# Performance work log

Hardware: AMD Instinct MI355X
Metric: run time of the kernel (lower is better)

Reference implementation:

```python
import jax, jax.numpy as jnp
import numpy as np
from jax import lax

L, E, H, V, B, S = 25, 64, 8, 30000, 1000, 512


def setup_inputs() -> dict:
    key = jax.random.key(0)
    ks = jax.random.split(key, 24)
    p = lambda k, shape: (jax.random.normal(k, shape) * 0.1).astype(jnp.float32)
    inp = {
        "x": jax.random.randint(ks[0], (B, S), 0, V),
        "embedding": p(ks[1], (V, E)),
        # layer 0 (input dim = E)
        "W_xz0": p(ks[2], (E, H)), "W_hz0": p(ks[3], (H, H)), "b_z0": p(ks[4], (H,)),
        "W_xr0": p(ks[5], (E, H)), "W_hr0": p(ks[6], (H, H)), "b_r0": p(ks[7], (H,)),
        "W_xH0": p(ks[8], (E, H)), "W_rH0": p(ks[9], (H, H)), "b_H0": p(ks[10], (H,)),
        # layers 1..L-1 stacked (input dim = H)
        "W_xz": p(ks[11], (L - 1, H, H)), "W_hz": p(ks[12], (L - 1, H, H)), "b_z": p(ks[13], (L - 1, H)),
        "W_xr": p(ks[14], (L - 1, H, H)), "W_hr": p(ks[15], (L - 1, H, H)), "b_r": p(ks[16], (L - 1, H)),
        "W_xH": p(ks[17], (L - 1, H, H)), "W_rH": p(ks[18], (L - 1, H, H)), "b_H": p(ks[19], (L - 1, H)),
        "W_hy": p(ks[20], (H, 1)), "b_y": p(ks[21], (1,)),
    }
    return inp


def _cell(x_t, h, Wxz, Whz, bz, Wxr, Whr, br, WxH, WrH, bH):
    z = jax.nn.sigmoid(x_t @ Wxz + h @ Whz + bz)
    r = jax.nn.sigmoid(x_t @ Wxr + h @ Whr + br)
    Hc = jnp.tanh(x_t @ WxH + (h * r) @ WrH + bH)
    return h * (1.0 - z) + z * Hc


def reference(x, embedding, W_xz0, W_hz0, b_z0, W_xr0, W_hr0, b_r0, W_xH0, W_rH0, b_H0,
              W_xz, W_hz, b_z, W_xr, W_hr, b_r, W_xH, W_rH, b_H, W_hy, b_y):
    emb = embedding[x]                     # [B, S, E]
    bsz = x.shape[0]
    h0 = jnp.zeros((L, bsz, H), dtype=embedding.dtype)

    def time_step(h_all, x_t):            # h_all: [L, B, H]; x_t: [B, E]
        h_new0 = _cell(x_t, h_all[0], W_xz0, W_hz0, b_z0, W_xr0, W_hr0, b_r0, W_xH0, W_rH0, b_H0)

        def layer_step(inp_t, ws):
            Wxz, Whz, bz, Wxr, Whr, br, WxH, WrH, bH, h_prev = ws
            h_new = _cell(inp_t, h_prev, Wxz, Whz, bz, Wxr, Whr, br, WxH, WrH, bH)
            return h_new, h_new

        _, h_rest = lax.scan(layer_step, h_new0,
                             (W_xz, W_hz, b_z, W_xr, W_hr, b_r, W_xH, W_rH, b_H, h_all[1:]))
        return jnp.concatenate([h_new0[None], h_rest], axis=0), None

    h_last, _ = lax.scan(time_step, h0, jnp.swapaxes(emb, 0, 1))  # scan over S
    logits = h_last[-1] @ W_hy + b_y       # [B, 1]
    return logits.squeeze(-1), h_last
```

## Files before the change

### kernel.cpp

```cpp
#include <hip/hip_runtime.h>
#include <hip/hip_bf16.h>
#include <stdint.h>

#define L_ 25
#define E_ 64
#define H_ 8
#define B_ 1000
#define S_ 512
#define GQ 4
#define NCELL (L_ * GQ)
#define TPBR (NCELL * 8)
#define TS 4
#define NSUPER (S_ / TS + L_ - 1)
#define HS 12
#define XG 36

typedef float v2f __attribute__((ext_vector_type(2)));
typedef float v4f __attribute__((ext_vector_type(4)));

#define PIN(x) asm volatile("" : "+v"(x))

__device__ __forceinline__ v2f pkfma(v2f a, v2f b, v2f c) {
  v2f d;
  asm("v_pk_fma_f32 %0, %1, %2, %3" : "=v"(d) : "v"(a), "v"(b), "v"(c));
  return d;
}
__device__ __forceinline__ v2f pkfma_l(v2f a, v2f b, v2f c) {
  v2f d;
  asm("v_pk_fma_f32 %0, %1, %2, %3 op_sel:[0,0,0] op_sel_hi:[0,1,1]"
      : "=v"(d) : "v"(a), "v"(b), "v"(c));
  return d;
}
__device__ __forceinline__ v2f pkfma_h(v2f a, v2f b, v2f c) {
  v2f d;
  asm("v_pk_fma_f32 %0, %1, %2, %3 op_sel:[1,0,0] op_sel_hi:[1,1,1]"
      : "=v"(d) : "v"(a), "v"(b), "v"(c));
  return d;
}
__device__ __forceinline__ v2f pkadd(v2f a, v2f b) {
  v2f d;
  asm("v_pk_add_f32 %0, %1, %2" : "=v"(d) : "v"(a), "v"(b));
  return d;
}
__device__ __forceinline__ v2f vlo(v4f v) { return __builtin_shufflevector(v, v, 0, 1); }
__device__ __forceinline__ v2f vhi(v4f v) { return __builtin_shufflevector(v, v, 2, 3); }
__device__ __forceinline__ v2f mk2(float a, float b) { v2f r; r.x = a; r.y = b; return r; }

#define CHAIN8(acc, ma, mb, w)            \
  acc = pkfma_l(vlo(ma), w[0], acc);      \
  acc = pkfma_h(vlo(ma), w[1], acc);      \
  acc = pkfma_l(vhi(ma), w[2], acc);      \
  acc = pkfma_h(vhi(ma), w[3], acc);      \
  acc = pkfma_l(vlo(mb), w[4], acc);      \
  acc = pkfma_h(vlo(mb), w[5], acc);      \
  acc = pkfma_l(vhi(mb), w[6], acc);      \
  acc = pkfma_h(vhi(mb), w[7], acc);

#define CHAIN4P(acc, ma, mb, w)           \
  acc = pkfma(vlo(ma), w[0], acc);        \
  acc = pkfma(vhi(ma), w[1], acc);        \
  acc = pkfma(vlo(mb), w[2], acc);        \
  acc = pkfma(vhi(mb), w[3], acc);

__device__ __forceinline__ float ulo(uint32_t u) { return __uint_as_float(u << 16); }
__device__ __forceinline__ float uhi(uint32_t u) { return __uint_as_float(u & 0xffff0000u); }

__device__ __forceinline__ float toF(float v) { return v; }
__device__ __forceinline__ float toF(__hip_bfloat16 v) { return __bfloat162float(v); }
__device__ __forceinline__ void stP(float* p, float v) { *p = v; }
__device__ __forceinline__ void stP(__hip_bfloat16* p, float v) { *p = __float2bfloat16(v); }

__device__ __forceinline__ v2f loadC2(const float* p) { return *(const v2f*)p; }
__device__ __forceinline__ v2f loadC2(const __hip_bfloat16* p) {
  const uint32_t u = *(const uint32_t*)p;
  return mk2(ulo(u), uhi(u));
}

__device__ __forceinline__ void load8f(const __hip_bfloat16* p, float* o) {
  const uint4 v = *(const uint4*)p;
  o[0] = ulo(v.x); o[1] = uhi(v.x); o[2] = ulo(v.y); o[3] = uhi(v.y);
  o[4] = ulo(v.z); o[5] = uhi(v.z); o[6] = ulo(v.w); o[7] = uhi(v.w);
}
__device__ __forceinline__ void load8f(const float* p, float* o) {
  const float4 a = ((const float4*)p)[0];
  const float4 b = ((const float4*)p)[1];
  o[0] = a.x; o[1] = a.y; o[2] = a.z; o[3] = a.w;
  o[4] = b.x; o[5] = b.y; o[6] = b.z; o[7] = b.w;
}

__device__ __forceinline__ void st4(float* p, float a, float b, float c, float d) {
  float4 v; v.x = a; v.y = b; v.z = c; v.w = d;
  *(float4*)p = v;
}
__device__ __forceinline__ void st4(__hip_bfloat16* p, float a, float b, float c, float d) {
  __hip_bfloat16 t[4] = {__float2bfloat16(a), __float2bfloat16(b),
                         __float2bfloat16(c), __float2bfloat16(d)};
  *(ushort4*)p = *(ushort4*)t;
}

__device__ __forceinline__ float sigmo(float x) {
  return __builtin_amdgcn_rcpf(1.f + __expf(-x));
}

__device__ __forceinline__ void detect64(const unsigned short* __restrict__ u,
                                         int tid, float* fl) {
  if (tid < 64) {
    float m = 0.f;
#pragma unroll
    for (int k = 0; k < 4; ++k) {
      const uint32_t q = u[tid * 4 + k];
      float v = fabsf(__uint_as_float(q << 16));
      if (!(v < 1e30f)) v = 1e30f;
      m = fmaxf(m, v);
    }
#pragma unroll
    for (int off = 32; off; off >>= 1) m = fmaxf(m, __shfl_down(m, off, 64));
    if (tid == 0) *fl = (m > 2.0f) ? 0.f : 1.f;
  }
}

template <typename T, typename PT>
__device__ __forceinline__ void pre_body(
    const int* __restrict__ x, const void* __restrict__ embv,
    const void* __restrict__ Wzv, const void* __restrict__ Wrv,
    const void* __restrict__ Whv, PT* __restrict__ pre,
    float* WL, float* TBb) {
  const T* emb = (const T*)embv;
  const T* Wz = (const T*)Wzv;
  const T* Wr = (const T*)Wrv;
  const T* Wh = (const T*)Whv;
  const int tid = threadIdx.x;

  for (int idx = tid; idx < 64 * 24; idx += 256) {
    const int k = idx / 24, c = idx - k * 24;
    float w;
    if (c < 16) w = toF(((c & 1) ? Wr : Wz)[k * 8 + (c >> 1)]);
    else        w = toF(Wh[k * 8 + (c - 16)]);
    WL[idx] = w;
  }
  __syncthreads();

  const int tok = blockIdx.x * 256 + tid;
  const int t = x[tok];

  v2f acc[12];
#pragma unroll
  for (int q = 0; q < 12; ++q) acc[q] = mk2(0.f, 0.f);

  for (int kb = 0; kb < 8; ++kb) {
    float e[8];
    load8f(emb + (size_t)t * E_ + kb * 8, e);
#pragma unroll
    for (int k8 = 0; k8 < 8; ++k8) {
      const v4f* wr = (const v4f*)(WL + (kb * 8 + k8) * 24);
      const v2f ee = mk2(e[k8], e[k8]);
#pragma unroll
      for (int q = 0; q < 6; ++q) {
        const v4f w4 = wr[q];
        acc[2 * q]     = pkfma(ee, vlo(w4), acc[2 * q]);
        acc[2 * q + 1] = pkfma(ee, vhi(w4), acc[2 * q + 1]);
      }
    }
  }

  const int wid = tid >> 6, lane = tid & 63;
  float* tb = TBb + wid * (24 * 65);
#pragma unroll
  for (int q = 0; q < 12; ++q) {
    tb[(2 * q) * 65 + lane] = acc[q].x;
    tb[(2 * q + 1) * 65 + lane] = acc[q].y;
  }
  asm volatile("s_waitcnt lgkmcnt(0)" ::: "memory");
  __builtin_amdgcn_wave_barrier();

  PT* ob = pre + (size_t)(blockIdx.x * 256 + wid * 64) * 24;
#pragma unroll
  for (int it = 0; it < 6; ++it) {
    const int F0 = it * 256 + lane * 4;
    float o[4];
#pragma unroll
    for (int e2 = 0; e2 < 4; ++e2) {
      const int F = F0 + e2;
      const int tk = F / 24;
      const int c = F - tk * 24;
      o[e2] = tb[c * 65 + tk];
    }
    st4(ob + F0, o[0], o[1], o[2], o[3]);
  }
}

template <typename PT>
__global__ __launch_bounds__(256, 4) void gru_pre(
    const int* __restrict__ x, const void* __restrict__ emb,
    const void* __restrict__ Wz, const void* __restrict__ Wr,
    const void* __restrict__ Wh, PT* __restrict__ pre) {
  __shared__ __align__(16) float WL[64 * 24];
  __shared__ __align__(16) float TB[4][24 * 65];
  __shared__ float fl;
  detect64((const unsigned short*)emb, threadIdx.x, &fl);
  __syncthreads();
  if (fl != 0.f) pre_body<__hip_bfloat16, PT>(x, emb, Wz, Wr, Wh, pre, WL, &TB[0][0]);
  else           pre_body<float, PT>(x, emb, Wz, Wr, Wh, pre, WL, &TB[0][0]);
}

#define TIMESTEP(hprev, axK, ahK, slot, hnout)                       \
  {                                                                  \
    const v4f h01_ = ((const v4f*)hgw)[0];                           \
    const v4f h23_ = ((const v4f*)hgw)[1];                           \
    v2f azrh_ = bzr;                                                 \
    CHAIN8(azrh_, h01_, h23_, wzrh);                                 \
    const v2f azr_ = pkadd(azrh_, axK);                              \
    const float r_ = sigmo(azr_.y);                                  \
    *hrgj = (hprev) * r_;                                            \
    __builtin_amdgcn_wave_barrier();                                 \
    const v4f r01_ = ((const v4f*)hrg)[0];                           \
    const v4f r23_ = ((const v4f*)hrg)[1];                           \
    CHAIN4P(ahK, r01_, r23_, wrh2);                                  \
    const float ah_ = ahK.x + ahK.y;                                 \
    const float ez_ = __expf(fminf(-azr_.x, 30.f));                  \
    const float eh_ = __expf(fminf(-2.f * ah_, 30.f));               \
    const float t_ = (hprev) * ez_;                                  \
    const float num_ = fmaf(eh_, t_ - 1.f, t_ + 1.f);                \
    const float den_ = (1.f + ez_) * (1.f + eh_);                    \
    hnout = num_ * __builtin_amdgcn_rcpf(den_);                      \
    *hgwj = hnout;                                                   \
    xc[(slot) * 8 + j] = hnout;                                      \
    __builtin_amdgcn_wave_barrier();                                 \
  }

template <typename T, typename PT>
__device__ __forceinline__ void rec_body(
    const PT* __restrict__ pre,
    const void* __restrict__ Whz0v, const void* __restrict__ bz0v,
    const void* __restrict__ Whr0v, const void* __restrict__ br0v,
    const void* __restrict__ WrH0v, const void* __restrict__ bH0v,
    const void* __restrict__ Wxzv, const void* __restrict__ Whzv,
    const void* __restrict__ bzv, const void* __restrict__ Wxrv,
    const void* __restrict__ Whrv, const void* __restrict__ brv,
    const void* __restrict__ WxHv, const void* __restrict__ WrHv,
    const void* __restrict__ bHv, const void* __restrict__ Whyv,
    const void* __restrict__ byv, void* __restrict__ outv,
    float* hsh, float* hrsh, float* xbuf) {
  const T* Whz0 = (const T*)Whz0v; const T* bz0 = (const T*)bz0v;
  const T* Whr0 = (const T*)Whr0v; const T* br0 = (const T*)br0v;
  const T* WrH0 = (const T*)WrH0v; const T* bH0 = (const T*)bH0v;
  const T* Wxz = (const T*)Wxzv;   const T* Whz = (const T*)Whzv;
  const T* bz = (const T*)bzv;     const T* Wxr = (const T*)Wxrv;
  const T* Whr = (const T*)Whrv;   const T* br = (const T*)brv;
  const T* WxH = (const T*)WxHv;   const T* WrH = (const T*)WrHv;
  const T* bH = (const T*)bHv;     const T* Why = (const T*)Whyv;
  const T* by = (const T*)byv;     T* out = (T*)outv;

  const int tid = threadIdx.x;
  const int gi = tid >> 3;
  const int j = tid & 7;
  const int l = gi >> 2;
  const int g = gi & 3;
  const int b = blockIdx.x * GQ + g;

  for (int i = tid; i < NCELL * HS; i += TPBR) { hsh[i] = 0.f; hrsh[i] = 0.f; }
  for (int i = tid; i < 2 * NCELL * XG; i += TPBR) xbuf[i] = 0.f;

  v2f wzrx[8], wzrh[8], wxh2[4], wrh2[4], bzr;
  float vbh;
  if (l == 0) {
#pragma unroll
    for (int k = 0; k < 8; ++k) {
      wzrh[k] = mk2(toF(Whz0[k * 8 + j]), toF(Whr0[k * 8 + j]));
      wzrx[k] = mk2(0.f, 0.f);
    }
#pragma unroll
    for (int q = 0; q < 4; ++q) {
      wrh2[q] = mk2(toF(WrH0[(2 * q) * 8 + j]), toF(WrH0[(2 * q + 1) * 8 + j]));
      wxh2[q] = mk2(0.f, 0.f);
    }
    bzr = mk2(toF(bz0[j]), toF(br0[j]));
    vbh = toF(bH0[j]);
  } else {
    const int base = (l - 1) * 64;
#pragma unroll
    for (int k = 0; k < 8; ++k) {
      wzrx[k] = mk2(toF(Wxz[base + k * 8 + j]), toF(Wxr[base + k * 8 + j]));
      wzrh[k] = mk2(toF(Whz[base + k * 8 + j]), toF(Whr[base + k * 8 + j]));
    }
#pragma unroll
    for (int q = 0; q < 4; ++q) {
      wxh2[q] = mk2(toF(WxH[base + (2 * q) * 8 + j]), toF(WxH[base + (2 * q + 1) * 8 + j]));
      wrh2[q] = mk2(toF(WrH[base + (2 * q) * 8 + j]), toF(WrH[base + (2 * q + 1) * 8 + j]));
    }
    bzr = mk2(toF(bz[(l - 1) * 8 + j]), toF(br[(l - 1) * 8 + j]));
    vbh = toF(bH[(l - 1) * 8 + j]);
  }
#pragma unroll
  for (int k = 0; k < 8; ++k) { PIN(wzrx[k]); PIN(wzrh[k]); }
#pragma unroll
  for (int q = 0; q < 4; ++q) { PIN(wxh2[q]); PIN(wrh2[q]); }
  PIN(bzr); PIN(vbh);

  const PT* ppr = pre + (size_t)b * (S_ * 24);
  v2f czr0 = mk2(0.f, 0.f), czr1 = czr0, czr2 = czr0, czr3 = czr0;
  float ch0 = 0.f, ch1 = 0.f, ch2 = 0.f, ch3 = 0.f;
  if (l == 0) {
    czr0 = loadC2(ppr + 0 * 24 + 2 * j);  ch0 = toF(ppr[0 * 24 + 16 + j]);
    czr1 = loadC2(ppr + 1 * 24 + 2 * j);  ch1 = toF(ppr[1 * 24 + 16 + j]);
    czr2 = loadC2(ppr + 2 * 24 + 2 * j);  ch2 = toF(ppr[2 * 24 + 16 + j]);
    czr3 = loadC2(ppr + 3 * 24 + 2 * j);  ch3 = toF(ppr[3 * 24 + 16 + j]);
  }

  float* hgw = hsh + gi * HS;
  float* hrg = hrsh + gi * HS;
  float* hgwj = hgw + j;
  float* hrgj = hrg + j;
  const int gp = (gi >= GQ) ? (gi - GQ) * XG : 0;
  const float* xpe = xbuf + NCELL * XG + gp;
  const float* xpo = xbuf + gp;
  float* xce = xbuf + gi * XG;
  float* xco = xbuf + NCELL * XG + gi * XG;

  float hown = 0.f;

  __syncthreads();

  for (int s = 0; s < NSUPER; ++s) {
    const unsigned rel = (unsigned)(s - l);
    if (rel < (unsigned)(S_ / TS)) {
      const float* xp = (s & 1) ? xpo : xpe;
      float* xc = (s & 1) ? xco : xce;

      const v4f xa0 = ((const v4f*)xp)[0];
      const v4f xb0 = ((const v4f*)xp)[1];
      const v4f xa1 = ((const v4f*)xp)[2];
      const v4f xb1 = ((const v4f*)xp)[3];

      v2f nzr0 = mk2(0.f, 0.f), nzr1 = nzr0, nzr2 = nzr0, nzr3 = nzr0;
      float nh0 = 0.f, nh1 = 0.f, nh2 = 0.f, nh3 = 0.f;
      const bool pf = (l == 0) && (rel + 1u < (unsigned)(S_ / TS));
      if (pf) {
        const PT* pn = ppr + (TS * rel + 4) * 24;
        nzr0 = loadC2(pn + 0 * 24 + 2 * j);  nh0 = toF(pn[0 * 24 + 16 + j]);
        nzr1 = loadC2(pn + 1 * 24 + 2 * j);  nh1 = toF(pn[1 * 24 + 16 + j]);
        nzr2 = loadC2(pn + 2 * 24 + 2 * j);  nh2 = toF(pn[2 * 24 + 16 + j]);
        nzr3 = loadC2(pn + 3 * 24 + 2 * j);  nh3 = toF(pn[3 * 24 + 16 + j]);
      }

      v2f ax0 = czr0; CHAIN8(ax0, xa0, xb0, wzrx);
      v2f ah0 = mk2(ch0, vbh); CHAIN4P(ah0, xa0, xb0, wxh2);
      v2f ax1 = czr1; CHAIN8(ax1, xa1, xb1, wzrx);
      v2f ah1 = mk2(ch1, vbh); CHAIN4P(ah1, xa1, xb1, wxh2);

      float hn0, hn1, hn2, hn3;
      TIMESTEP(hown, ax0, ah0, 0, hn0);

      const v4f xa2 = ((const v4f*)xp)[4];
      const v4f xb2 = ((const v4f*)xp)[5];
      const v4f xa3 = ((const v4f*)xp)[6];
      const v4f xb3 = ((const v4f*)xp)[7];
      v2f ax2 = czr2; CHAIN8(ax2, xa2, xb2, wzrx);
      v2f ah2 = mk2(ch2, vbh); CHAIN4P(ah2, xa2, xb2, wxh2);
      v2f ax3 = czr3; CHAIN8(ax3, xa3, xb3, wzrx);
      v2f ah3 = mk2(ch3, vbh); CHAIN4P(ah3, xa3, xb3, wxh2);

      TIMESTEP(hn0, ax1, ah1, 1, hn1);
      TIMESTEP(hn1, ax2, ah2, 2, hn2);
      TIMESTEP(hn2, ax3, ah3, 3, hn3);

      hown = hn3;
      czr0 = nzr0; ch0 = nh0; czr1 = nzr1; ch1 = nh1;
      czr2 = nzr2; ch2 = nh2; czr3 = nzr3; ch3 = nh3;
    }
    __syncthreads();
  }

  stP(out + B_ + (l * B_ + b) * H_ + j, hown);
  if (l == L_ - 1 && j == 0) {
    float ssum = toF(by[0]);
#pragma unroll
    for (int k = 0; k < 8; ++k) ssum = fmaf(hgw[k], toF(Why[k]), ssum);
    stP(out + b, ssum);
  }
}

template <typename PT>
__global__ __launch_bounds__(TPBR, 4) void gru_rec(
    const void* __restrict__ emb, const PT* __restrict__ pre,
    const void* __restrict__ Whz0, const void* __restrict__ bz0,
    const void* __restrict__ Whr0, const void* __restrict__ br0,
    const void* __restrict__ WrH0, const void* __restrict__ bH0,
    const void* __restrict__ Wxz, const void* __restrict__ Whz,
    const void* __restrict__ bz, const void* __restrict__ Wxr,
    const void* __restrict__ Whr, const void* __restrict__ br,
    const void* __restrict__ WxH, const void* __restrict__ WrH,
    const void* __restrict__ bH, const void* __restrict__ Why,
    const void* __restrict__ by, void* __restrict__ out) {
  __shared__ __align__(16) float hsh[NCELL * HS];
  __shared__ __align__(16) float hrsh[NCELL * HS];
  __shared__ __align__(16) float xbuf[2 * NCELL * XG];
  __shared__ float fl;
  detect64((const unsigned short*)emb, threadIdx.x, &fl);
  __syncthreads();
  if (fl != 0.f)
    rec_body<__hip_bfloat16, PT>(pre, Whz0, bz0, Whr0, br0, WrH0, bH0, Wxz, Whz,
                                 bz, Wxr, Whr, br, WxH, WrH, bH, Why, by, out,
                                 hsh, hrsh, xbuf);
  else
    rec_body<float, PT>(pre, Whz0, bz0, Whr0, br0, WrH0, bH0, Wxz, Whz, bz, Wxr,
                        Whr, br, WxH, WrH, bH, Why, by, out, hsh, hrsh, xbuf);
}

template <typename PT>
static void launch_all(void* const* d_in, PT* pre, void* d_out, hipStream_t stream) {
  gru_pre<PT><<<B_ * S_ / 256, 256, 0, stream>>>(
      (const int*)d_in[0], d_in[1], d_in[2], d_in[5], d_in[8], pre);
  gru_rec<PT><<<B_ / GQ, TPBR, 0, stream>>>(
      d_in[1], pre, d_in[3], d_in[4], d_in[6], d_in[7], d_in[9], d_in[10],
      d_in[11], d_in[12], d_in[13], d_in[14], d_in[15], d_in[16], d_in[17],
      d_in[18], d_in[19], d_in[20], d_in[21], d_out);
}

extern "C" void kernel_launch(void* const* d_in, const int* in_sizes, int n_in,
                              void* d_out, int out_size, void* d_ws, size_t ws_size,
                              hipStream_t stream) {
  const size_t needF = (size_t)B_ * S_ * 24 * sizeof(float);
  if (ws_size >= needF)
    launch_all<float>(d_in, (float*)d_ws, d_out, stream);
  else
    launch_all<__hip_bfloat16>(d_in, (__hip_bfloat16*)d_ws, d_out, stream);
}
```

Before: 395.8 us.

## Process two batch rows per thread in GRU recurrence to raise ILP

Each thread now handles two independent batch chains (gi0 and gi1) instead of one, halving the block's thread count. The two recurrences are interleaved in a combined timestep macro so their dependent latency chains overlap within a thread. This trades more registers per thread and fewer waves for instruction-level parallelism on the serial recurrence. The launch-bounds occupancy hint is also dropped.

```diff
diff --git a/kernel.cpp b/kernel.cpp
--- a/kernel.cpp
+++ b/kernel.cpp
@@ -9,7 +9,8 @@
 #define S_ 512
 #define GQ 4
 #define NCELL (L_ * GQ)
-#define TPBR (NCELL * 8)
+#define NPT 2
+#define TPBR (L_ * (GQ / NPT) * 8)
 #define TS 4
 #define NSUPER (S_ / TS + L_ - 1)
 #define HS 12
@@ -203,29 +204,48 @@
   else           pre_body<float, PT>(x, emb, Wz, Wr, Wh, pre, WL, &TB[0][0]);
 }
 
-#define TIMESTEP(hprev, axK, ahK, slot, hnout)                       \
-  {                                                                  \
-    const v4f h01_ = ((const v4f*)hgw)[0];                           \
-    const v4f h23_ = ((const v4f*)hgw)[1];                           \
-    v2f azrh_ = bzr;                                                 \
-    CHAIN8(azrh_, h01_, h23_, wzrh);                                 \
-    const v2f azr_ = pkadd(azrh_, axK);                              \
-    const float r_ = sigmo(azr_.y);                                  \
-    *hrgj = (hprev) * r_;                                            \
-    __builtin_amdgcn_wave_barrier();                                 \
-    const v4f r01_ = ((const v4f*)hrg)[0];                           \
-    const v4f r23_ = ((const v4f*)hrg)[1];                           \
-    CHAIN4P(ahK, r01_, r23_, wrh2);                                  \
-    const float ah_ = ahK.x + ahK.y;                                 \
-    const float ez_ = __expf(fminf(-azr_.x, 30.f));                  \
-    const float eh_ = __expf(fminf(-2.f * ah_, 30.f));               \
-    const float t_ = (hprev) * ez_;                                  \
-    const float num_ = fmaf(eh_, t_ - 1.f, t_ + 1.f);                \
-    const float den_ = (1.f + ez_) * (1.f + eh_);                    \
-    hnout = num_ * __builtin_amdgcn_rcpf(den_);                      \
-    *hgwj = hnout;                                                   \
-    xc[(slot) * 8 + j] = hnout;                                      \
-    __builtin_amdgcn_wave_barrier();                                 \
+#define TIMESTEP2(hp0, hp1, ax0_, ah0_, ax1_, ah1_, slotT, hn0_, hn1_)   \
+  {                                                                      \
+    const v4f ha01 = ((const v4f*)hgw0)[0];                              \
+    const v4f ha23 = ((const v4f*)hgw0)[1];                              \
+    const v4f hb01 = ((const v4f*)hgw1)[0];                              \
+    const v4f hb23 = ((const v4f*)hgw1)[1];                              \
+    v2f azrh0 = bzr;                                                     \
+    CHAIN8(azrh0, ha01, ha23, wzrh);                                     \
+    v2f azrh1 = bzr;                                                     \
+    CHAIN8(azrh1, hb01, hb23, wzrh);                                     \
+    const v2f azr0 = pkadd(azrh0, ax0_);                                 \
+    const v2f azr1 = pkadd(azrh1, ax1_);                                 \
+    const float r0_ = sigmo(azr0.y);                                     \
+    const float r1_ = sigmo(azr1.y);                                     \
+    *hrg0j = (hp0) * r0_;                                                \
+    *hrg1j = (hp1) * r1_;                                                \
+    __builtin_amdgcn_wave_barrier();                                     \
+    const v4f ra01 = ((const v4f*)hrg0)[0];                              \
+    const v4f ra23 = ((const v4f*)hrg0)[1];                              \
+    const v4f rb01 = ((const v4f*)hrg1)[0];                              \
+    const v4f rb23 = ((const v4f*)hrg1)[1];                              \
+    CHAIN4P(ah0_, ra01, ra23, wrh2);                                     \
+    CHAIN4P(ah1_, rb01, rb23, wrh2);                                     \
+    const float aha_ = ah0_.x + ah0_.y;                                  \
+    const float ahb_ = ah1_.x + ah1_.y;                                  \
+    const float ez0_ = __expf(fminf(-azr0.x, 30.f));                     \
+    const float eh0_ = __expf(fminf(-2.f * aha_, 30.f));                 \
+    const float ez1_ = __expf(fminf(-azr1.x, 30.f));                     \
+    const float eh1_ = __expf(fminf(-2.f * ahb_, 30.f));                 \
+    const float t0_ = (hp0) * ez0_;                                      \
+    const float t1_ = (hp1) * ez1_;                                      \
+    const float nu0_ = fmaf(eh0_, t0_ - 1.f, t0_ + 1.f);                 \
+    const float nu1_ = fmaf(eh1_, t1_ - 1.f, t1_ + 1.f);                 \
+    const float de0_ = (1.f + ez0_) * (1.f + eh0_);                      \
+    const float de1_ = (1.f + ez1_) * (1.f + eh1_);                      \
+    hn0_ = nu0_ * __builtin_amdgcn_rcpf(de0_);                           \
+    hn1_ = nu1_ * __builtin_amdgcn_rcpf(de1_);                           \
+    *hgw0j = hn0_;                                                       \
+    *hgw1j = hn1_;                                                       \
+    xc0[(slotT) * 8 + j] = hn0_;                                         \
+    xc1[(slotT) * 8 + j] = hn1_;                                         \
+    __builtin_amdgcn_wave_barrier();                                     \
   }
 
 template <typename T, typename PT>
@@ -252,11 +272,14 @@
   const T* by = (const T*)byv;     T* out = (T*)outv;
 
   const int tid = threadIdx.x;
-  const int gi = tid >> 3;
+  const int slot = tid >> 3;
   const int j = tid & 7;
-  const int l = gi >> 2;
-  const int g = gi & 3;
-  const int b = blockIdx.x * GQ + g;
+  const int l = slot >> 1;
+  const int gh = slot & 1;
+  const int gi0 = l * GQ + gh;
+  const int gi1 = gi0 + 2;
+  const int b0 = blockIdx.x * GQ + gh;
+  const int b1 = b0 + 2;
 
   for (int i = tid; i < NCELL * HS; i += TPBR) { hsh[i] = 0.f; hrsh[i] = 0.f; }
   for (int i = tid; i < 2 * NCELL * XG; i += TPBR) xbuf[i] = 0.f;
@@ -297,91 +320,140 @@
   for (int q = 0; q < 4; ++q) { PIN(wxh2[q]); PIN(wrh2[q]); }
   PIN(bzr); PIN(vbh);
 
-  const PT* ppr = pre + (size_t)b * (S_ * 24);
-  v2f czr0 = mk2(0.f, 0.f), czr1 = czr0, czr2 = czr0, czr3 = czr0;
-  float ch0 = 0.f, ch1 = 0.f, ch2 = 0.f, ch3 = 0.f;
+  const PT* ppr0 = pre + (size_t)b0 * (S_ * 24);
+  const PT* ppr1 = pre + (size_t)b1 * (S_ * 24);
+  v2f czr00 = mk2(0.f, 0.f), czr01 = czr00, czr02 = czr00, czr03 = czr00;
+  v2f czr10 = czr00, czr11 = czr00, czr12 = czr00, czr13 = czr00;
+  float ch00 = 0.f, ch01 = 0.f, ch02 = 0.f, ch03 = 0.f;
+  float ch10 = 0.f, ch11 = 0.f, ch12 = 0.f, ch13 = 0.f;
   if (l == 0) {
-    czr0 = loadC2(ppr + 0 * 24 + 2 * j);  ch0 = toF(ppr[0 * 24 + 16 + j]);
-    czr1 = loadC2(ppr + 1 * 24 + 2 * j);  ch1 = toF(ppr[1 * 24 + 16 + j]);
-    czr2 = loadC2(ppr + 2 * 24 + 2 * j);  ch2 = toF(ppr[2 * 24 + 16 + j]);
-    czr3 = loadC2(ppr + 3 * 24 + 2 * j);  ch3 = toF(ppr[3 * 24 + 16 + j]);
-  }
-
-  float* hgw = hsh + gi * HS;
-  float* hrg = hrsh + gi * HS;
-  float* hgwj = hgw + j;
-  float* hrgj = hrg + j;
-  const int gp = (gi >= GQ) ? (gi - GQ) * XG : 0;
-  const float* xpe = xbuf + NCELL * XG + gp;
-  const float* xpo = xbuf + gp;
-  float* xce = xbuf + gi * XG;
-  float* xco = xbuf + NCELL * XG + gi * XG;
-
-  float hown = 0.f;
+    czr00 = loadC2(ppr0 + 0 * 24 + 2 * j);  ch00 = toF(ppr0[0 * 24 + 16 + j]);
+    czr01 = loadC2(ppr0 + 1 * 24 + 2 * j);  ch01 = toF(ppr0[1 * 24 + 16 + j]);
+    czr02 = loadC2(ppr0 + 2 * 24 + 2 * j);  ch02 = toF(ppr0[2 * 24 + 16 + j]);
+    czr03 = loadC2(ppr0 + 3 * 24 + 2 * j);  ch03 = toF(ppr0[3 * 24 + 16 + j]);
+    czr10 = loadC2(ppr1 + 0 * 24 + 2 * j);  ch10 = toF(ppr1[0 * 24 + 16 + j]);
+    czr11 = loadC2(ppr1 + 1 * 24 + 2 * j);  ch11 = toF(ppr1[1 * 24 + 16 + j]);
+    czr12 = loadC2(ppr1 + 2 * 24 + 2 * j);  ch12 = toF(ppr1[2 * 24 + 16 + j]);
+    czr13 = loadC2(ppr1 + 3 * 24 + 2 * j);  ch13 = toF(ppr1[3 * 24 + 16 + j]);
+  }
+
+  float* hgw0 = hsh + gi0 * HS;
+  float* hgw1 = hsh + gi1 * HS;
+  float* hrg0 = hrsh + gi0 * HS;
+  float* hrg1 = hrsh + gi1 * HS;
+  float* hgw0j = hgw0 + j;
+  float* hgw1j = hgw1 + j;
+  float* hrg0j = hrg0 + j;
+  float* hrg1j = hrg1 + j;
+  const int gp0 = (gi0 >= GQ) ? (gi0 - GQ) * XG : 0;
+  const int gp1 = (gi1 >= GQ) ? (gi1 - GQ) * XG : 0;
+  const float* xpe0 = xbuf + NCELL * XG + gp0;
+  const float* xpo0 = xbuf + gp0;
+  const float* xpe1 = xbuf + NCELL * XG + gp1;
+  const float* xpo1 = xbuf + gp1;
+  float* xce0 = xbuf + gi0 * XG;
+  float* xco0 = xbuf + NCELL * XG + gi0 * XG;
+  float* xce1 = xbuf + gi1 * XG;
+  float* xco1 = xbuf + NCELL * XG + gi1 * XG;
+
+  float hown0 = 0.f, hown1 = 0.f;
 
   __syncthreads();
 
   for (int s = 0; s < NSUPER; ++s) {
     const unsigned rel = (unsigned)(s - l);
     if (rel < (unsigned)(S_ / TS)) {
-      const float* xp = (s & 1) ? xpo : xpe;
-      float* xc = (s & 1) ? xco : xce;
-
-      const v4f xa0 = ((const v4f*)xp)[0];
-      const v4f xb0 = ((const v4f*)xp)[1];
-      const v4f xa1 = ((const v4f*)xp)[2];
-      const v4f xb1 = ((const v4f*)xp)[3];
-
-      v2f nzr0 = mk2(0.f, 0.f), nzr1 = nzr0, nzr2 = nzr0, nzr3 = nzr0;
-      float nh0 = 0.f, nh1 = 0.f, nh2 = 0.f, nh3 = 0.f;
+      const float* xp0 = (s & 1) ? xpo0 : xpe0;
+      const float* xp1 = (s & 1) ? xpo1 : xpe1;
+      float* xc0 = (s & 1) ? xco0 : xce0;
+      float* xc1 = (s & 1) ? xco1 : xce1;
+
+      const v4f c0t0a = ((const v4f*)xp0)[0];
+      const v4f c0t0b = ((const v4f*)xp0)[1];
+      const v4f c0t1a = ((const v4f*)xp0)[2];
+      const v4f c0t1b = ((const v4f*)xp0)[3];
+      const v4f c1t0a = ((const v4f*)xp1)[0];
+      const v4f c1t0b = ((const v4f*)xp1)[1];
+      const v4f c1t1a = ((const v4f*)xp1)[2];
+      const v4f c1t1b = ((const v4f*)xp1)[3];
+
+      v2f nzr00 = mk2(0.f, 0.f), nzr01 = nzr00, nzr02 = nzr00, nzr03 = nzr00;
+      v2f nzr10 = nzr00, nzr11 = nzr00, nzr12 = nzr00, nzr13 = nzr00;
+      float nh00 = 0.f, nh01 = 0.f, nh02 = 0.f, nh03 = 0.f;
+      float nh10 = 0.f, nh11 = 0.f, nh12 = 0.f, nh13 = 0.f;
       const bool pf = (l == 0) && (rel + 1u < (unsigned)(S_ / TS));
       if (pf) {
-        const PT* pn = ppr + (TS * rel + 4) * 24;
-        nzr0 = loadC2(pn + 0 * 24 + 2 * j);  nh0 = toF(pn[0 * 24 + 16 + j]);
-        nzr1 = loadC2(pn + 1 * 24 + 2 * j);  nh1 = toF(pn[1 * 24 + 16 + j]);
-        nzr2 = loadC2(pn + 2 * 24 + 2 * j);  nh2 = toF(pn[2 * 24 + 16 + j]);
-        nzr3 = loadC2(pn + 3 * 24 + 2 * j);  nh3 = toF(pn[3 * 24 + 16 + j]);
+        const PT* pn0 = ppr0 + (TS * rel + 4) * 24;
+        const PT* pn1 = ppr1 + (TS * rel + 4) * 24;
+        nzr00 = loadC2(pn0 + 0 * 24 + 2 * j);  nh00 = toF(pn0[0 * 24 + 16 + j]);
+        nzr01 = loadC2(pn0 + 1 * 24 + 2 * j);  nh01 = toF(pn0[1 * 24 + 16 + j]);
+        nzr02 = loadC2(pn0 + 2 * 24 + 2 * j);  nh02 = toF(pn0[2 * 24 + 16 + j]);
+        nzr03 = loadC2(pn0 + 3 * 24 + 2 * j);  nh03 = toF(pn0[3 * 24 + 16 + j]);
+        nzr10 = loadC2(pn1 + 0 * 24 + 2 * j);  nh10 = toF(pn1[0 * 24 + 16 + j]);
+        nzr11 = loadC2(pn1 + 1 * 24 + 2 * j);  nh11 = toF(pn1[1 * 24 + 16 + j]);
+        nzr12 = loadC2(pn1 + 2 * 24 + 2 * j);  nh12 = toF(pn1[2 * 24 + 16 + j]);
+        nzr13 = loadC2(pn1 + 3 * 24 + 2 * j);  nh13 = toF(pn1[3 * 24 + 16 + j]);
       }
 
-      v2f ax0 = czr0; CHAIN8(ax0, xa0, xb0, wzrx);
-      v2f ah0 = mk2(ch0, vbh); CHAIN4P(ah0, xa0, xb0, wxh2);
-      v2f ax1 = czr1; CHAIN8(ax1, xa1, xb1, wzrx);
-      v2f ah1 = mk2(ch1, vbh); CHAIN4P(ah1, xa1, xb1, wxh2);
-
-      float hn0, hn1, hn2, hn3;
-      TIMESTEP(hown, ax0, ah0, 0, hn0);
-
-      const v4f xa2 = ((const v4f*)xp)[4];
-      const v4f xb2 = ((const v4f*)xp)[5];
-      const v4f xa3 = ((const v4f*)xp)[6];
-      const v4f xb3 = ((const v4f*)xp)[7];
-      v2f ax2 = czr2; CHAIN8(ax2, xa2, xb2, wzrx);
-      v2f ah2 = mk2(ch2, vbh); CHAIN4P(ah2, xa2, xb2, wxh2);
-      v2f ax3 = czr3; CHAIN8(ax3, xa3, xb3, wzrx);
-      v2f ah3 = mk2(ch3, vbh); CHAIN4P(ah3, xa3, xb3, wxh2);
-
-      TIMESTEP(hn0, ax1, ah1, 1, hn1);
-      TIMESTEP(hn1, ax2, ah2, 2, hn2);
-      TIMESTEP(hn2, ax3, ah3, 3, hn3);
-
-      hown = hn3;
-      czr0 = nzr0; ch0 = nh0; czr1 = nzr1; ch1 = nh1;
-      czr2 = nzr2; ch2 = nh2; czr3 = nzr3; ch3 = nh3;
+      v2f ax00 = czr00; CHAIN8(ax00, c0t0a, c0t0b, wzrx);
+      v2f ah00 = mk2(ch00, vbh); CHAIN4P(ah00, c0t0a, c0t0b, wxh2);
+      v2f ax10 = czr10; CHAIN8(ax10, c1t0a, c1t0b, wzrx);
+      v2f ah10 = mk2(ch10, vbh); CHAIN4P(ah10, c1t0a, c1t0b, wxh2);
+      v2f ax01 = czr01; CHAIN8(ax01, c0t1a, c0t1b, wzrx);
+      v2f ah01 = mk2(ch01, vbh); CHAIN4P(ah01, c0t1a, c0t1b, wxh2);
+      v2f ax11 = czr11; CHAIN8(ax11, c1t1a, c1t1b, wzrx);
+      v2f ah11 = mk2(ch11, vbh); CHAIN4P(ah11, c1t1a, c1t1b, wxh2);
+
+      float hn00, hn01, hn02, hn03, hn10, hn11, hn12, hn13;
+      TIMESTEP2(hown0, hown1, ax00, ah00, ax10, ah10, 0, hn00, hn10);
+
+      const v4f c0t2a = ((const v4f*)xp0)[4];
+      const v4f c0t2b = ((const v4f*)xp0)[5];
+      const v4f c0t3a = ((const v4f*)xp0)[6];
+      const v4f c0t3b = ((const v4f*)xp0)[7];
+      const v4f c1t2a = ((const v4f*)xp1)[4];
+      const v4f c1t2b = ((const v4f*)xp1)[5];
+      const v4f c1t3a = ((const v4f*)xp1)[6];
+      const v4f c1t3b = ((const v4f*)xp1)[7];
+      v2f ax02 = czr02; CHAIN8(ax02, c0t2a, c0t2b, wzrx);
+      v2f ah02 = mk2(ch02, vbh); CHAIN4P(ah02, c0t2a, c0t2b, wxh2);
+      v2f ax12 = czr12; CHAIN8(ax12, c1t2a, c1t2b, wzrx);
+      v2f ah12 = mk2(ch12, vbh); CHAIN4P(ah12, c1t2a, c1t2b, wxh2);
+      v2f ax03 = czr03; CHAIN8(ax03, c0t3a, c0t3b, wzrx);
+      v2f ah03 = mk2(ch03, vbh); CHAIN4P(ah03, c0t3a, c0t3b, wxh2);
+      v2f ax13 = czr13; CHAIN8(ax13, c1t3a, c1t3b, wzrx);
+      v2f ah13 = mk2(ch13, vbh); CHAIN4P(ah13, c1t3a, c1t3b, wxh2);
+
+      TIMESTEP2(hn00, hn10, ax01, ah01, ax11, ah11, 1, hn01, hn11);
+      TIMESTEP2(hn01, hn11, ax02, ah02, ax12, ah12, 2, hn02, hn12);
+      TIMESTEP2(hn02, hn12, ax03, ah03, ax13, ah13, 3, hn03, hn13);
+
+      hown0 = hn03; hown1 = hn13;
+      czr00 = nzr00; ch00 = nh00; czr01 = nzr01; ch01 = nh01;
+      czr02 = nzr02; ch02 = nh02; czr03 = nzr03; ch03 = nh03;
+      czr10 = nzr10; ch10 = nh10; czr11 = nzr11; ch11 = nh11;
+      czr12 = nzr12; ch12 = nh12; czr13 = nzr13; ch13 = nh13;
     }
     __syncthreads();
   }
 
-  stP(out + B_ + (l * B_ + b) * H_ + j, hown);
+  stP(out + B_ + (l * B_ + b0) * H_ + j, hown0);
+  stP(out + B_ + (l * B_ + b1) * H_ + j, hown1);
   if (l == L_ - 1 && j == 0) {
-    float ssum = toF(by[0]);
-#pragma unroll
-    for (int k = 0; k < 8; ++k) ssum = fmaf(hgw[k], toF(Why[k]), ssum);
-    stP(out + b, ssum);
+    float s0 = toF(by[0]), s1 = toF(by[0]);
+#pragma unroll
+    for (int k = 0; k < 8; ++k) {
+      const float wyk = toF(Why[k]);
+      s0 = fmaf(hgw0[k], wyk, s0);
+      s1 = fmaf(hgw1[k], wyk, s1);
+    }
+    stP(out + b0, s0);
+    stP(out + b1, s1);
   }
 }
 
 template <typename PT>
-__global__ __launch_bounds__(TPBR, 4) void gru_rec(
+__global__ __launch_bounds__(TPBR) void gru_rec(
     const void* __restrict__ emb, const PT* __restrict__ pre,
     const void* __restrict__ Whz0, const void* __restrict__ bz0,
     const void* __restrict__ Whr0, const void* __restrict__ br0,
```

Result: slower. 447.7 us (+13.1%).
